# Optimization experiments

Measured on AMD Instinct MI355X. Metric: run time of the kernel, lower is better.

The kernel has to match this reference:

```python
import jax, jax.numpy as jnp
import numpy as np

U, N, C, D, E, K, NS = 100000, 50000, 20, 128, 1000000, 50000, 9


def setup_inputs() -> dict:
    key = jax.random.key(0)
    ks = jax.random.split(key, 13)
    s = 0.1  # embedding init scale
    return {
        "user_emb": jax.random.normal(ks[0], (U, D), jnp.float32) * s,
        "news_emb": jax.random.normal(ks[1], (N, D), jnp.float32) * s,
        "cat_emb": jax.random.normal(ks[2], (C, D), jnp.float32) * s,
        "cx": jax.random.normal(ks[3], (U, D), jnp.float32) * s,
        "W_ih": jax.random.normal(ks[4], (4 * D, D), jnp.float32) * (1.0 / np.sqrt(D)),
        "W_hh": jax.random.normal(ks[5], (4 * D, D), jnp.float32) * (1.0 / np.sqrt(D)),
        "b_ih": jax.random.normal(ks[6], (4 * D,), jnp.float32) * (1.0 / np.sqrt(D)),
        "b_hh": jax.random.normal(ks[7], (4 * D,), jnp.float32) * (1.0 / np.sqrt(D)),
        "edge_src": jax.random.randint(ks[8], (E,), 0, N, jnp.int32),
        "edge_dst": jax.random.randint(ks[9], (E,), 0, U, jnp.int32),
        "edge_cat": jax.random.randint(ks[10], (E,), 0, C, jnp.int32),
        "ns_idx": jax.random.randint(ks[11], (K, NS), 0, N, jnp.int32),
        "user_score_idx": jax.random.randint(ks[12], (K,), 0, U, jnp.int32),
    }


def reference(user_emb, news_emb, cat_emb, cx, W_ih, W_hh, b_ih, b_hh,
              edge_src, edge_dst, edge_cat, ns_idx, user_score_idx):
    # --- GCN message passing (DGL send_and_recv on 'clicked_reverse': news -> user) ---
    # per-edge message: src news embedding * category (edge) embedding
    msg = news_emb[edge_src] * cat_emb[edge_cat]                      # [E, D]
    agg = jax.ops.segment_sum(msg, edge_dst, num_segments=U)          # [U, D]
    cnt = jax.ops.segment_sum(jnp.ones_like(msg[:, 0]), edge_dst, num_segments=U)
    mean_msg = agg / jnp.maximum(cnt, 1.0)[:, None]                   # mailbox mean
    x = user_emb + mean_msg                                           # residual add -> LSTM input

    # --- LSTMCell (PyTorch gate order i, f, g, o), prev h = original user_emb ---
    gates = x @ W_ih.T + b_ih + user_emb @ W_hh.T + b_hh              # [U, 4D]
    i, f, g, o = jnp.split(gates, 4, axis=-1)
    c_new = jax.nn.sigmoid(f) * cx + jax.nn.sigmoid(i) * jnp.tanh(g)
    h_new = jax.nn.sigmoid(o) * jnp.tanh(c_new)                       # updated user node_emb

    # --- candidate scoring: (user * news_cand).sum(-1) over 9 candidates ---
    cand_u = h_new[user_score_idx]                                    # [K, D]
    cand_n = news_emb[ns_idx]                                         # [K, 9, D]
    score = jnp.einsum('kd,knd->kn', cand_u, cand_n)                  # [K, 9]
    return score
```

## Files before the change

kernel.cpp:

```cpp
#include <hip/hip_runtime.h>
#include <math.h>

#define U_CNT 100000
#define N_CNT 50000
#define C_CNT 20
#define D_DIM 128
#define E_CNT 1000000
#define K_CNT 50000
#define NS_CNT 9
#define CAP 64

#define BM 64
#define NBLK 1563

#define OFF_CNT    0
#define OFF_BPT    400384
#define OFF_BSUM   662528
#define OFF_NBF    665600
#define OFF_BUCKET 13465600
#define OFF_ABF    39065664

typedef __attribute__((ext_vector_type(8))) short bf16x8;
typedef __attribute__((ext_vector_type(4))) float f32x4;

__device__ __forceinline__ unsigned short f2bf(float f) {
    unsigned u = __builtin_bit_cast(unsigned, f);
    u = (u + 0x7FFF + ((u >> 16) & 1)) >> 16;
    return (unsigned short)u;
}
__device__ __forceinline__ float bf2f(unsigned short b) {
    return __builtin_bit_cast(float, (unsigned)b << 16);
}

__device__ __forceinline__ float sig_fast(float x) {
    float t = __builtin_amdgcn_exp2f(x * -1.44269504f);
    return __builtin_amdgcn_rcpf(1.f + t);
}
__device__ __forceinline__ float tanh_fast(float x) {
    x = fminf(fmaxf(x, -15.f), 15.f);
    float t = __builtin_amdgcn_exp2f(x * 2.88539008f);
    return (t - 1.f) * __builtin_amdgcn_rcpf(t + 1.f);
}

__device__ __forceinline__ void gload16(const void* g, void* l) {
    __builtin_amdgcn_global_load_lds(
        (const __attribute__((address_space(1))) unsigned int*)g,
        (__attribute__((address_space(3))) unsigned int*)l, 16, 0, 0);
}

__global__ void k_zero(int* __restrict__ cnt) {
    int i = blockIdx.x * 256 + threadIdx.x;
    if (i < U_CNT) cnt[i] = 0;
}

__global__ void k_prep(const float* __restrict__ Wih, const float* __restrict__ Whh,
                       const float* __restrict__ bih, const float* __restrict__ bhh,
                       unsigned short* __restrict__ Bpt, float* __restrict__ bsum_p) {
    int idx = blockIdx.x * 256 + threadIdx.x;
    if (idx < 512) {
        int dim = idx >> 2, g = idx & 3;
        bsum_p[idx] = bih[g * 128 + dim] + bhh[g * 128 + dim];
    }
    if (idx >= 512 * 256) return;
    int col = idx >> 8, kp = idx & 255;
    int seg = kp >> 6, gst = (kp >> 3) & 7, e = kp & 7;
    int k = seg * 64 + (gst ^ (col & 7)) * 8 + e;
    int d = col >> 2, g = col & 3;
    int j = g * 128 + d;
    float v = (k < 128) ? Wih[j * 128 + k] : Whh[j * 128 + (k - 128)];
    Bpt[idx] = f2bf(v);
}

__global__ void k_nbf(const float* __restrict__ news, unsigned short* __restrict__ nbf) {
    int i = blockIdx.x * 256 + threadIdx.x;
    if (i >= N_CNT * 32) return;
    float4 v = ((const float4*)news)[i];
    ushort4 o = {f2bf(v.x), f2bf(v.y), f2bf(v.z), f2bf(v.w)};
    ((ushort4*)nbf)[i] = o;
}

__global__ void k_bucket(const int* __restrict__ dst, const int* __restrict__ esrc,
                         const int* __restrict__ ecat, int* __restrict__ cnt,
                         int* __restrict__ bucket) {
    int e = blockIdx.x * 256 + threadIdx.x;
    if (e >= E_CNT) return;
    int d = dst[e];
    int slot = atomicAdd(&cnt[d], 1);
    if (slot < CAP) bucket[d * CAP + slot] = (esrc[e] & 0xFFFF) | (ecat[e] << 16);
}

__global__ void k_agg(const float* __restrict__ user_emb,
                      const unsigned short* __restrict__ news_bf,
                      const float* __restrict__ cat_emb,
                      const int* __restrict__ cnt,
                      const int* __restrict__ bucket,
                      unsigned short* __restrict__ Abf) {
    int wid  = (blockIdx.x * blockDim.x + threadIdx.x) >> 6;
    int lane = threadIdx.x & 63;
    if (wid >= U_CNT) return;
    int deg = cnt[wid];
    if (deg > CAP) deg = CAP;
    int half = lane >> 5, lid = lane & 31;
    const int* bp = bucket + wid * CAP;
    float4 acc = {0.f, 0.f, 0.f, 0.f};
    int trips = (deg + 1) >> 1;
    int p = 0; float vmask = 0.f;
    if (trips > 0) {
        int e0 = half;
        p = bp[e0 < deg ? e0 : 0];
        vmask = (e0 < deg) ? 1.f : 0.f;
    }
    for (int t = 0; t < trips; ++t) {
        int en = 2 * (t + 1) + half;
        int pn = 0; float vn = 0.f;
        if (t + 1 < trips) {
            pn = bp[en < deg ? en : 0];
            vn = (en < deg) ? 1.f : 0.f;
        }
        int s = p & 0xFFFF;
        int c = p >> 16;
        ushort4 nv = *(const ushort4*)&news_bf[(size_t)s * 128 + lid * 4];
        float4  cv = *(const float4*)&cat_emb[c * 128 + lid * 4];
        acc.x += vmask * bf2f(nv.x) * cv.x;
        acc.y += vmask * bf2f(nv.y) * cv.y;
        acc.z += vmask * bf2f(nv.z) * cv.z;
        acc.w += vmask * bf2f(nv.w) * cv.w;
        p = pn; vmask = vn;
    }
    acc.x += __shfl_xor(acc.x, 32, 64);
    acc.y += __shfl_xor(acc.y, 32, 64);
    acc.z += __shfl_xor(acc.z, 32, 64);
    acc.w += __shfl_xor(acc.w, 32, 64);
    if (half == 0) {
        float inv = 1.0f / (float)(deg < 1 ? 1 : deg);
        float4 ue = *(const float4*)&user_emb[(size_t)wid * 128 + lid * 4];
        float4 xv = {ue.x + acc.x * inv, ue.y + acc.y * inv,
                     ue.z + acc.z * inv, ue.w + acc.w * inv};
        int seg = lid >> 4;
        int gr  = (lid >> 1) & 7;
        int eo  = (lid & 1) * 4;
        int pos = seg * 64 + ((gr ^ (wid & 7)) * 8) + eo;
        size_t base = (size_t)wid * 256;
        ushort4 xb = {f2bf(xv.x), f2bf(xv.y), f2bf(xv.z), f2bf(xv.w)};
        ushort4 ub = {f2bf(ue.x), f2bf(ue.y), f2bf(ue.z), f2bf(ue.w)};
        *(ushort4*)&Abf[base + pos] = xb;
        *(ushort4*)&Abf[base + 128 + pos] = ub;
    }
}

#define STAGE(K0, BUF)                                                                   \
    {                                                                                    \
        int bg3 = ((K0) >> 3) & 7;                                                       \
        int seg64 = ((K0) >> 6) * 64;                                                    \
        char* Ab_ = smem + (BUF) * 4096;                                                 \
        char* Bb_ = smem + 8192 + (BUF) * 32768;                                         \
        _Pragma("unroll")                                                                \
        for (int ii = 0; ii < 5; ++ii) {                                                 \
            int inst = w + ii * 8;                                                       \
            if (inst < 4) {                                                              \
                int row = inst * 16 + (l >> 2);                                          \
                int kg = (l & 3) ^ (row & 3);                                            \
                gload16(Abf + (size_t)(u0 + row) * 256 + seg64 +                         \
                            ((bg3 + kg) ^ (row & 7)) * 8,                                \
                        Ab_ + inst * 1024 + l * 16);                                     \
            } else if (inst < 36) {                                                      \
                int b = inst - 4;                                                        \
                int col = b * 16 + (l >> 2);                                             \
                int kg = (l & 3) ^ (col & 3);                                            \
                gload16(Bpt + (size_t)col * 256 + seg64 +                                \
                            ((bg3 + kg) ^ (col & 7)) * 8,                                \
                        Bb_ + b * 1024 + l * 16);                                        \
            }                                                                            \
        }                                                                                \
    }

__global__ __launch_bounds__(512, 4) void k_gemm_lstm(
    const unsigned short* __restrict__ Abf, const unsigned short* __restrict__ Bpt,
    const float* __restrict__ bsum_p, const float* __restrict__ cx,
    unsigned short* __restrict__ hout)
{
    __shared__ __align__(16) char smem[73728];
    int t = threadIdx.x, l = t & 63, w = t >> 6;
    int u0 = blockIdx.x * BM;
    int wn0 = w * 64;

    f32x4 acc[4][4];
#pragma unroll
    for (int m = 0; m < 4; ++m)
#pragma unroll
        for (int n = 0; n < 4; ++n) acc[m][n] = (f32x4){0.f, 0.f, 0.f, 0.f};

    STAGE(0, 0);
    __syncthreads();

#pragma unroll
    for (int step = 0; step < 8; ++step) {
        int cur = step & 1;
        if (step < 7) STAGE((step + 1) * 32, cur ^ 1);
        const char* Ab = smem + cur * 4096;
        const char* Bb = smem + 8192 + cur * 32768;
        int kg = l >> 4;
        bf16x8 af[4], bfr[4];
#pragma unroll
        for (int m = 0; m < 4; ++m) {
            int row = m * 16 + (l & 15);
            af[m] = *(const bf16x8*)(Ab + row * 64 + ((kg ^ (row & 3)) * 16));
        }
#pragma unroll
        for (int n = 0; n < 4; ++n) {
            int col = wn0 + n * 16 + (l & 15);
            bfr[n] = *(const bf16x8*)(Bb + col * 64 + ((kg ^ (col & 3)) * 16));
        }
#pragma unroll
        for (int m = 0; m < 4; ++m)
#pragma unroll
            for (int n = 0; n < 4; ++n)
                acc[m][n] = __builtin_amdgcn_mfma_f32_16x16x32_bf16(
                    af[m], bfr[n], acc[m][n], 0, 0, 0);
        __syncthreads();
    }

    float* gbuf = (float*)smem;
#pragma unroll
    for (int mm = 0; mm < 2; ++mm) {
#pragma unroll
        for (int mo = 0; mo < 2; ++mo) {
#pragma unroll
            for (int n = 0; n < 4; ++n)
#pragma unroll
                for (int r = 0; r < 4; ++r)
                    gbuf[(mo * 16 + (l >> 4) * 4 + r) * 516 + wn0 + n * 16 + (l & 15)] =
                        acc[mm * 2 + mo][n][r];
        }
        __syncthreads();
#pragma unroll
        for (int i = 0; i < 8; ++i) {
            int c = t + 512 * i;
            int row = c >> 7, dim = c & 127;
            int u = u0 + mm * 32 + row;
            if (u < U_CNT) {
                float4 gv = *(const float4*)&gbuf[row * 516 + dim * 4];
                float4 bs = *(const float4*)&bsum_p[dim * 4];
                float I = gv.x + bs.x, F = gv.y + bs.y, G = gv.z + bs.z, O = gv.w + bs.w;
                float cxv = cx[(size_t)u * 128 + dim];
                float cn = sig_fast(F) * cxv + sig_fast(I) * tanh_fast(G);
                hout[(size_t)u * 256 + dim] = f2bf(sig_fast(O) * tanh_fast(cn));
            }
        }
        __syncthreads();
    }
}

__global__ void k_score(const unsigned short* __restrict__ hbf,
                        const unsigned short* __restrict__ nbf,
                        const int* __restrict__ ns_idx, const int* __restrict__ usi,
                        float* __restrict__ out) {
    int gh  = (blockIdx.x * 256 + threadIdx.x) >> 5;
    int lid = threadIdx.x & 31;
    if (gh >= K_CNT) return;
    int u = usi[gh];
    ushort4 hv = *(const ushort4*)&hbf[(size_t)u * 256 + lid * 4];
    float h0 = bf2f(hv.x), h1 = bf2f(hv.y), h2 = bf2f(hv.z), h3 = bf2f(hv.w);
    const int* np = ns_idx + gh * 9;
    float val = 0.f;
#pragma unroll
    for (int j = 0; j < 9; ++j) {
        int n = np[j];
        ushort4 nv = *(const ushort4*)&nbf[(size_t)n * 128 + lid * 4];
        float p = h0 * bf2f(nv.x) + h1 * bf2f(nv.y) + h2 * bf2f(nv.z) + h3 * bf2f(nv.w);
#pragma unroll
        for (int off = 16; off; off >>= 1) p += __shfl_xor(p, off, 64);
        if (lid == j) val = p;
    }
    if (lid < 9) out[(size_t)gh * 9 + lid] = val;
}

extern "C" void kernel_launch(void* const* d_in, const int* in_sizes, int n_in,
                              void* d_out, int out_size, void* d_ws, size_t ws_size,
                              hipStream_t stream) {
    const float* user_emb = (const float*)d_in[0];
    const float* news_emb = (const float*)d_in[1];
    const float* cat_emb  = (const float*)d_in[2];
    const float* cx       = (const float*)d_in[3];
    const float* W_ih     = (const float*)d_in[4];
    const float* W_hh     = (const float*)d_in[5];
    const float* b_ih     = (const float*)d_in[6];
    const float* b_hh     = (const float*)d_in[7];
    const int* edge_src   = (const int*)d_in[8];
    const int* edge_dst   = (const int*)d_in[9];
    const int* edge_cat   = (const int*)d_in[10];
    const int* ns_idx     = (const int*)d_in[11];
    const int* usi        = (const int*)d_in[12];
    float* out = (float*)d_out;

    char* ws = (char*)d_ws;
    int*            cnt    = (int*)(ws + OFF_CNT);
    unsigned short* Bpt    = (unsigned short*)(ws + OFF_BPT);
    float*          bsum_p = (float*)(ws + OFF_BSUM);
    unsigned short* nbf    = (unsigned short*)(ws + OFF_NBF);
    int*            bucket = (int*)(ws + OFF_BUCKET);
    unsigned short* Abf    = (unsigned short*)(ws + OFF_ABF);
    unsigned short* hbf    = (unsigned short*)(ws + OFF_ABF);

    k_zero<<<(U_CNT + 255) / 256, 256, 0, stream>>>(cnt);
    k_prep<<<512, 256, 0, stream>>>(W_ih, W_hh, b_ih, b_hh, Bpt, bsum_p);
    k_nbf<<<6250, 256, 0, stream>>>(news_emb, nbf);
    k_bucket<<<(E_CNT + 255) / 256, 256, 0, stream>>>(edge_dst, edge_src, edge_cat, cnt, bucket);
    k_agg<<<25000, 256, 0, stream>>>(user_emb, nbf, cat_emb, cnt, bucket, Abf);
    k_gemm_lstm<<<NBLK, 512, 0, stream>>>(Abf, Bpt, bsum_p, cx, hbf);
    k_score<<<(K_CNT * 32 + 255) / 256, 256, 0, stream>>>(hbf, nbf, ns_idx, usi, out);
}
```

Baseline: 427.3 us.

## Split LSTM GEMM across two N-halves per row tile with wider K stages

Each 64-row tile of the fused GEMM+LSTM kernel is now split into two blocks, each computing 256 of the 512 gate columns. This doubles the grid and halves the accumulator registers per thread. The K loop now runs in 4 stages of 64 elements instead of 8 of 32, with a new XOR swizzle and an explicit vmcnt wait before the first barrier. The output h is written compactly (stride 128) into the bucket region instead of overwriting Abf, which removes the aliasing hazard. The cost is that the A tile is now loaded twice from memory.

After: 401.6 us. 6.0% less time.

```diff
diff --git a/kernel.cpp b/kernel.cpp
--- a/kernel.cpp
+++ b/kernel.cpp
@@ -11,7 +11,7 @@
 #define CAP 64
 
 #define BM 64
-#define NBLK 1563
+#define NB2 3126
 
 #define OFF_CNT    0
 #define OFF_BPT    400384
@@ -148,27 +148,21 @@
     }
 }
 
-#define STAGE(K0, BUF)                                                                   \
+#define STAGE(S, BUF)                                                                    \
     {                                                                                    \
-        int bg3 = ((K0) >> 3) & 7;                                                       \
-        int seg64 = ((K0) >> 6) * 64;                                                    \
-        char* Ab_ = smem + (BUF) * 4096;                                                 \
-        char* Bb_ = smem + 8192 + (BUF) * 32768;                                         \
+        char* Ab_ = smem + (BUF) * 8192;                                                 \
+        char* Bb_ = smem + 16384 + (BUF) * 32768;                                        \
         _Pragma("unroll")                                                                \
         for (int ii = 0; ii < 5; ++ii) {                                                 \
-            int inst = w + ii * 8;                                                       \
-            if (inst < 4) {                                                              \
-                int row = inst * 16 + (l >> 2);                                          \
-                int kg = (l & 3) ^ (row & 3);                                            \
-                gload16(Abf + (size_t)(u0 + row) * 256 + seg64 +                         \
-                            ((bg3 + kg) ^ (row & 7)) * 8,                                \
+            int inst = w * 5 + ii;                                                       \
+            if (inst < 8) {                                                              \
+                int row = inst * 8 + (l >> 3);                                           \
+                gload16(Abf + (size_t)(u0 + row) * 256 + (S) * 64 + (l & 7) * 8,         \
                         Ab_ + inst * 1024 + l * 16);                                     \
-            } else if (inst < 36) {                                                      \
-                int b = inst - 4;                                                        \
-                int col = b * 16 + (l >> 2);                                             \
-                int kg = (l & 3) ^ (col & 3);                                            \
-                gload16(Bpt + (size_t)col * 256 + seg64 +                                \
-                            ((bg3 + kg) ^ (col & 7)) * 8,                                \
+            } else {                                                                     \
+                int b = inst - 8;                                                        \
+                int gcol = n0 + b * 8 + (l >> 3);                                        \
+                gload16(Bpt + (size_t)gcol * 256 + (S) * 64 + (l & 7) * 8,               \
                         Bb_ + b * 1024 + l * 16);                                        \
             }                                                                            \
         }                                                                                \
@@ -177,77 +171,75 @@
 __global__ __launch_bounds__(512, 4) void k_gemm_lstm(
     const unsigned short* __restrict__ Abf, const unsigned short* __restrict__ Bpt,
     const float* __restrict__ bsum_p, const float* __restrict__ cx,
-    unsigned short* __restrict__ hout)
+    unsigned short* __restrict__ hbf)
 {
-    __shared__ __align__(16) char smem[73728];
+    __shared__ __align__(16) char smem[81920];
     int t = threadIdx.x, l = t & 63, w = t >> 6;
-    int u0 = blockIdx.x * BM;
-    int wn0 = w * 64;
-
-    f32x4 acc[4][4];
+    int mb = blockIdx.x >> 1, nb = blockIdx.x & 1;
+    int u0 = mb * BM;
+    int n0 = nb * 256;
+    int wn0 = w * 32;
+
+    f32x4 acc[4][2];
 #pragma unroll
     for (int m = 0; m < 4; ++m)
 #pragma unroll
-        for (int n = 0; n < 4; ++n) acc[m][n] = (f32x4){0.f, 0.f, 0.f, 0.f};
+        for (int n = 0; n < 2; ++n) acc[m][n] = (f32x4){0.f, 0.f, 0.f, 0.f};
 
     STAGE(0, 0);
+    asm volatile("s_waitcnt vmcnt(0)" ::: "memory");
     __syncthreads();
 
 #pragma unroll
-    for (int step = 0; step < 8; ++step) {
+    for (int step = 0; step < 4; ++step) {
         int cur = step & 1;
-        if (step < 7) STAGE((step + 1) * 32, cur ^ 1);
-        const char* Ab = smem + cur * 4096;
-        const char* Bb = smem + 8192 + cur * 32768;
-        int kg = l >> 4;
-        bf16x8 af[4], bfr[4];
-#pragma unroll
-        for (int m = 0; m < 4; ++m) {
-            int row = m * 16 + (l & 15);
-            af[m] = *(const bf16x8*)(Ab + row * 64 + ((kg ^ (row & 3)) * 16));
-        }
-#pragma unroll
-        for (int n = 0; n < 4; ++n) {
-            int col = wn0 + n * 16 + (l & 15);
-            bfr[n] = *(const bf16x8*)(Bb + col * 64 + ((kg ^ (col & 3)) * 16));
-        }
-#pragma unroll
-        for (int m = 0; m < 4; ++m)
-#pragma unroll
-            for (int n = 0; n < 4; ++n)
-                acc[m][n] = __builtin_amdgcn_mfma_f32_16x16x32_bf16(
-                    af[m], bfr[n], acc[m][n], 0, 0, 0);
-        __syncthreads();
-    }
-
-    float* gbuf = (float*)smem;
-#pragma unroll
-    for (int mm = 0; mm < 2; ++mm) {
-#pragma unroll
-        for (int mo = 0; mo < 2; ++mo) {
-#pragma unroll
-            for (int n = 0; n < 4; ++n)
-#pragma unroll
-                for (int r = 0; r < 4; ++r)
-                    gbuf[(mo * 16 + (l >> 4) * 4 + r) * 516 + wn0 + n * 16 + (l & 15)] =
-                        acc[mm * 2 + mo][n][r];
+        if (step < 3) STAGE(step + 1, cur ^ 1);
+        const char* Ab = smem + cur * 8192;
+        const char* Bb = smem + 16384 + cur * 32768;
+#pragma unroll
+        for (int kf = 0; kf < 2; ++kf) {
+            int swz = ((kf * 4 + (l >> 4)) ^ (l & 7)) * 16;
+            bf16x8 af[4], bfr[2];
+#pragma unroll
+            for (int m = 0; m < 4; ++m)
+                af[m] = *(const bf16x8*)(Ab + (m * 16 + (l & 15)) * 128 + swz);
+#pragma unroll
+            for (int n = 0; n < 2; ++n)
+                bfr[n] = *(const bf16x8*)(Bb + (wn0 + n * 16 + (l & 15)) * 128 + swz);
+#pragma unroll
+            for (int m = 0; m < 4; ++m)
+#pragma unroll
+                for (int n = 0; n < 2; ++n)
+                    acc[m][n] = __builtin_amdgcn_mfma_f32_16x16x32_bf16(
+                        af[m], bfr[n], acc[m][n], 0, 0, 0);
         }
         __syncthreads();
-#pragma unroll
-        for (int i = 0; i < 8; ++i) {
-            int c = t + 512 * i;
-            int row = c >> 7, dim = c & 127;
-            int u = u0 + mm * 32 + row;
-            if (u < U_CNT) {
-                float4 gv = *(const float4*)&gbuf[row * 516 + dim * 4];
-                float4 bs = *(const float4*)&bsum_p[dim * 4];
-                float I = gv.x + bs.x, F = gv.y + bs.y, G = gv.z + bs.z, O = gv.w + bs.w;
-                float cxv = cx[(size_t)u * 128 + dim];
-                float cn = sig_fast(F) * cxv + sig_fast(I) * tanh_fast(G);
-                hout[(size_t)u * 256 + dim] = f2bf(sig_fast(O) * tanh_fast(cn));
-            }
+    }
+
+    float* gbuf = (float*)smem;
+#pragma unroll
+    for (int m = 0; m < 4; ++m)
+#pragma unroll
+        for (int n = 0; n < 2; ++n)
+#pragma unroll
+            for (int r = 0; r < 4; ++r)
+                gbuf[(m * 16 + (l >> 4) * 4 + r) * 260 + wn0 + n * 16 + (l & 15)] =
+                    acc[m][n][r];
+    __syncthreads();
+#pragma unroll
+    for (int i = 0; i < 8; ++i) {
+        int c = t + 512 * i;
+        int row = c >> 6, dloc = c & 63;
+        int u = u0 + row;
+        if (u < U_CNT) {
+            int gdim = nb * 64 + dloc;
+            float4 gv = *(const float4*)&gbuf[row * 260 + dloc * 4];
+            float4 bs = *(const float4*)&bsum_p[gdim * 4];
+            float I = gv.x + bs.x, F = gv.y + bs.y, G = gv.z + bs.z, O = gv.w + bs.w;
+            float cxv = cx[(size_t)u * 128 + gdim];
+            float cn = sig_fast(F) * cxv + sig_fast(I) * tanh_fast(G);
+            hbf[(size_t)u * 128 + gdim] = f2bf(sig_fast(O) * tanh_fast(cn));
         }
-        __syncthreads();
     }
 }
 
@@ -259,7 +251,7 @@
     int lid = threadIdx.x & 31;
     if (gh >= K_CNT) return;
     int u = usi[gh];
-    ushort4 hv = *(const ushort4*)&hbf[(size_t)u * 256 + lid * 4];
+    ushort4 hv = *(const ushort4*)&hbf[(size_t)u * 128 + lid * 4];
     float h0 = bf2f(hv.x), h1 = bf2f(hv.y), h2 = bf2f(hv.z), h3 = bf2f(hv.w);
     const int* np = ns_idx + gh * 9;
     float val = 0.f;
@@ -300,13 +292,13 @@
     unsigned short* nbf    = (unsigned short*)(ws + OFF_NBF);
     int*            bucket = (int*)(ws + OFF_BUCKET);
     unsigned short* Abf    = (unsigned short*)(ws + OFF_ABF);
-    unsigned short* hbf    = (unsigned short*)(ws + OFF_ABF);
+    unsigned short* hbf    = (unsigned short*)(ws + OFF_BUCKET);
 
     k_zero<<<(U_CNT + 255) / 256, 256, 0, stream>>>(cnt);
     k_prep<<<512, 256, 0, stream>>>(W_ih, W_hh, b_ih, b_hh, Bpt, bsum_p);
     k_nbf<<<6250, 256, 0, stream>>>(news_emb, nbf);
     k_bucket<<<(E_CNT + 255) / 256, 256, 0, stream>>>(edge_dst, edge_src, edge_cat, cnt, bucket);
     k_agg<<<25000, 256, 0, stream>>>(user_emb, nbf, cat_emb, cnt, bucket, Abf);
-    k_gemm_lstm<<<NBLK, 512, 0, stream>>>(Abf, Bpt, bsum_p, cx, hbf);
+    k_gemm_lstm<<<NB2, 512, 0, stream>>>(Abf, Bpt, bsum_p, cx, hbf);
     k_score<<<(K_CNT * 32 + 255) / 256, 256, 0, stream>>>(hbf, nbf, ns_idx, usi, out);
 }
```
